# Kernel tuning notes

Hardware: AMD Instinct MI355X
Metric: run time of the kernel (lower is better)

## Reference

```python
import jax, jax.numpy as jnp
import numpy as np

B, S, D, H = 16, 4096, 1024, 1024
VOCAB = 512
EMB_DIM = 3


def setup_inputs() -> dict:
    key = jax.random.key(0)
    ks = jax.random.split(key, 12)
    sd = 1.0 / np.sqrt(D)
    sh = 1.0 / np.sqrt(H)
    return {
        "hs": jax.random.normal(ks[0], (B, S, D), dtype=jnp.float32),
        "ht_k": jax.random.normal(ks[1], (B, D), dtype=jnp.float32),
        "hm_k": jax.random.normal(ks[2], (B, H), dtype=jnp.float32),
        "Ws_w": jax.random.uniform(ks[3], (H, D), jnp.float32, -sd, sd),
        "Ws_b": jax.random.uniform(ks[4], (H,), jnp.float32, -sd, sd),
        "Wt_w": jax.random.uniform(ks[5], (H, D), jnp.float32, -sd, sd),
        "Wt_b": jax.random.uniform(ks[6], (H,), jnp.float32, -sd, sd),
        "Wr_w": jax.random.uniform(ks[7], (H, H), jnp.float32, -sh, sh),
        "Wr_b": jax.random.uniform(ks[8], (H,), jnp.float32, -sh, sh),
        "We_w": jax.random.uniform(ks[9], (H,), jnp.float32, -sh, sh),
        "We_b": jax.random.uniform(ks[10], (1,), jnp.float32, -sh, sh),
        "emb_table": jax.random.normal(ks[11], (VOCAB * VOCAB, EMB_DIM), dtype=jnp.float32),
        "entity_lambda": jnp.array([0.3, 0.5, 0.2], dtype=jnp.float32),
        "hs_i": jax.random.randint(jax.random.fold_in(key, 100), (B, S), 0, VOCAB),
        "ht_k_i": jax.random.randint(jax.random.fold_in(key, 101), (B,), 0, VOCAB),
    }


def reference(hs, ht_k, hm_k, Ws_w, Ws_b, Wt_w, Wt_b, Wr_w, Wr_b, We_w, We_b,
              emb_table, entity_lambda, hs_i, ht_k_i):
    # Projections
    W_hs = jnp.einsum('bsd,hd->bsh', hs, Ws_w) + Ws_b          # [B,S,H]
    W_ht = (ht_k @ Wt_w.T + Wt_b)[:, None, :]                   # [B,1,H]
    W_hm = (hm_k @ Wr_w.T + Wr_b)[:, None, :]                   # [B,1,H]
    # Additive attention score
    W_sum = jnp.tanh(W_hs + W_ht + W_hm) @ We_w + We_b[0]       # [B,S]
    # Relative-position bias: gather then contract with lambda
    rel_pos = hs_i * VOCAB + ht_k_i[:, None]                    # [B,S]
    rel_value = emb_table[rel_pos] @ entity_lambda              # [B,S]
    W_sum = W_sum + rel_value
    # Softmax over sequence, weighted sum of projected source states
    W_softmax = jax.nn.softmax(W_sum, axis=1)                   # [B,S]
    alpha = jnp.einsum('bs,bsh->bh', W_softmax, W_hs)           # [B,H]
    return alpha
```

## Files before the change

### kernel.cpp

```cpp
#include <hip/hip_runtime.h>
#include <hip/hip_bf16.h>
#include <cstdint>
#include <cstddef>

typedef __attribute__((ext_vector_type(4))) float f32x4;
typedef __attribute__((ext_vector_type(8))) short short8;

#define S_LEN 4096
#define D_DIM 1024
#define H_DIM 1024
#define B_SZ  16
#define M_TOT (B_SZ * S_LEN)
#define NT 32

__device__ __forceinline__ unsigned short f2bf(float f) {
  unsigned int u = __float_as_uint(f);
  u += 0x7fffu + ((u >> 16) & 1u);
  return (unsigned short)(u >> 16);
}

__device__ __forceinline__ void gload_lds16(void* lds, const void* g) {
  __builtin_amdgcn_global_load_lds(
      (const __attribute__((address_space(1))) unsigned int*)g,
      (__attribute__((address_space(3))) unsigned int*)lds, 16, 0, 0);
}

__device__ __forceinline__ float tanh_fast(float x) {
  return 1.0f - 2.0f / (1.0f + __expf(2.0f * x));
}

__global__ void cvt_hs_kernel(const float* __restrict__ w,
                              unsigned short* __restrict__ o) {
  size_t i = ((size_t)blockIdx.x * 256 + threadIdx.x) * 8;
  float4 v0 = *(const float4*)(w + i);
  float4 v1 = *(const float4*)(w + i + 4);
  union { unsigned short us[8]; short8 v; } pk;
  pk.us[0] = f2bf(v0.x); pk.us[1] = f2bf(v0.y);
  pk.us[2] = f2bf(v0.z); pk.us[3] = f2bf(v0.w);
  pk.us[4] = f2bf(v1.x); pk.us[5] = f2bf(v1.y);
  pk.us[6] = f2bf(v1.z); pk.us[7] = f2bf(v1.w);
  *(short8*)(o + i) = pk.v;
}

__global__ void cvt_w_kernel(const float* __restrict__ w,
                             unsigned short* __restrict__ o) {
  int i = (blockIdx.x * 256 + threadIdx.x) * 8;
  float4 v0 = *(const float4*)(w + i);
  float4 v1 = *(const float4*)(w + i + 4);
  union { unsigned short us[8]; short8 v; } pk;
  pk.us[0] = f2bf(v0.x); pk.us[1] = f2bf(v0.y);
  pk.us[2] = f2bf(v0.z); pk.us[3] = f2bf(v0.w);
  pk.us[4] = f2bf(v1.x); pk.us[5] = f2bf(v1.y);
  pk.us[6] = f2bf(v1.z); pk.us[7] = f2bf(v1.w);
  *(short8*)(o + i) = pk.v;
}

__global__ void prep_c_kernel(const float* __restrict__ ht,
                              const float* __restrict__ hm,
                              const float* __restrict__ Wt_w,
                              const float* __restrict__ Wt_b,
                              const float* __restrict__ Wr_w,
                              const float* __restrict__ Wr_b,
                              float* __restrict__ cvec) {
  int gw = blockIdx.x * 4 + (threadIdx.x >> 6);
  int lane = threadIdx.x & 63;
  int b = gw >> 10;
  int h = gw & 1023;
  const float* a1 = ht + b * D_DIM;
  const float* w1 = Wt_w + (size_t)h * D_DIM;
  const float* a2 = hm + b * H_DIM;
  const float* w2 = Wr_w + (size_t)h * H_DIM;
  float acc = 0.f;
#pragma unroll
  for (int i = 0; i < 4; ++i) {
    int d = lane * 4 + i * 256;
    float4 x1 = *(const float4*)(a1 + d);
    float4 y1 = *(const float4*)(w1 + d);
    float4 x2 = *(const float4*)(a2 + d);
    float4 y2 = *(const float4*)(w2 + d);
    acc += x1.x * y1.x + x1.y * y1.y + x1.z * y1.z + x1.w * y1.w;
    acc += x2.x * y2.x + x2.y * y2.y + x2.z * y2.z + x2.w * y2.w;
  }
#pragma unroll
  for (int off = 32; off >= 1; off >>= 1) acc += __shfl_xor(acc, off);
  if (lane == 0) cvec[b * H_DIM + h] = acc + Wt_b[h] + Wr_b[h];
}

__device__ __forceinline__ void issue_tile(int kt, int tid,
                                           unsigned short* lA,
                                           unsigned short* lB,
                                           const unsigned short* pA0,
                                           const unsigned short* pA1,
                                           const unsigned short* pB0,
                                           const unsigned short* pB1) {
  int bq = (kt & 3) * 8192;
  size_t ko = (size_t)kt * 32;
  gload_lds16(&lA[bq + tid * 8], pA0 + ko);
  gload_lds16(&lA[bq + 4096 + tid * 8], pA1 + ko);
  gload_lds16(&lB[bq + tid * 8], pB0 + ko);
  gload_lds16(&lB[bq + 4096 + tid * 8], pB1 + ko);
}

__device__ __forceinline__ void compute_tile(const unsigned short* bufA,
                                             const unsigned short* bufB,
                                             const int* aoff, const int* boff,
                                             f32x4 (&acc)[8][4]) {
  short8 bfr[4];
#pragma unroll
  for (int ni = 0; ni < 4; ++ni)
    bfr[ni] = *(const short8*)(bufB + boff[ni]);
  short8 af[4];
#pragma unroll
  for (int mi = 0; mi < 4; ++mi)
    af[mi] = *(const short8*)(bufA + aoff[mi]);
  __builtin_amdgcn_s_setprio(1);
#pragma unroll
  for (int mi = 0; mi < 4; ++mi)
#pragma unroll
    for (int ni = 0; ni < 4; ++ni)
      acc[mi][ni] = __builtin_amdgcn_mfma_f32_16x16x32_bf16(
          af[mi], bfr[ni], acc[mi][ni], 0, 0, 0);
  __builtin_amdgcn_s_setprio(0);
#pragma unroll
  for (int mi = 0; mi < 4; ++mi)
    af[mi] = *(const short8*)(bufA + aoff[4 + mi]);
  __builtin_amdgcn_s_setprio(1);
#pragma unroll
  for (int mi = 0; mi < 4; ++mi)
#pragma unroll
    for (int ni = 0; ni < 4; ++ni)
      acc[4 + mi][ni] = __builtin_amdgcn_mfma_f32_16x16x32_bf16(
          af[mi], bfr[ni], acc[4 + mi][ni], 0, 0, 0);
  __builtin_amdgcn_s_setprio(0);
}

__global__ __launch_bounds__(512, 2) void score_gemm2_kernel(
    const unsigned short* __restrict__ hsb,
    const unsigned short* __restrict__ Wsb,
    const float* __restrict__ cvec,
    const float* __restrict__ We_w,
    float* __restrict__ score_part) {
  extern __shared__ unsigned short dynls[];
  unsigned short* lA = dynls;
  unsigned short* lB = dynls + 4 * 8192;
  __shared__ float scorebuf[4][256];

  const int tid = threadIdx.x;
  const int lane = tid & 63;
  const int wave = tid >> 6;
  const int wm = wave >> 2;
  const int wn = wave & 3;
  const int l15 = lane & 15;
  const int lg = lane >> 4;

  int d = blockIdx.x;
  int tileid = (d & 7) * 128 + (d >> 3);
  const int mtile = tileid >> 2;
  const int nc = tileid & 3;
  const int m0 = mtile * 256;
  const int n0 = nc * 256;
  const int b = m0 >> 12;

  const int r0 = tid >> 2;
  const int r1 = 128 + r0;
  const int sp = tid & 3;
  const int c0 = (sp ^ ((r0 >> 1) & 3)) * 8;
  const int c1 = (sp ^ ((r1 >> 1) & 3)) * 8;
  const unsigned short* pA0 = hsb + (size_t)(m0 + r0) * D_DIM + c0;
  const unsigned short* pA1 = hsb + (size_t)(m0 + r1) * D_DIM + c1;
  const unsigned short* pB0 = Wsb + (size_t)(n0 + r0) * D_DIM + c0;
  const unsigned short* pB1 = Wsb + (size_t)(n0 + r1) * D_DIM + c1;

  int aoff[8], boff[4];
#pragma unroll
  for (int mi = 0; mi < 8; ++mi) {
    int row = wm * 128 + mi * 16 + l15;
    aoff[mi] = row * 32 + (lg ^ ((row >> 1) & 3)) * 8;
  }
#pragma unroll
  for (int ni = 0; ni < 4; ++ni) {
    int row = wn * 64 + ni * 16 + l15;
    boff[ni] = row * 32 + (lg ^ ((row >> 1) & 3)) * 8;
  }

  f32x4 acc[8][4];
#pragma unroll
  for (int i = 0; i < 8; ++i)
#pragma unroll
    for (int j = 0; j < 4; ++j) acc[i][j] = (f32x4){0.f, 0.f, 0.f, 0.f};

  issue_tile(0, tid, lA, lB, pA0, pA1, pB0, pB1);
  issue_tile(1, tid, lA, lB, pA0, pA1, pB0, pB1);
  issue_tile(2, tid, lA, lB, pA0, pA1, pB0, pB1);
  asm volatile("s_waitcnt vmcnt(8)\n\ts_barrier" ::: "memory");

  for (int kt = 0; kt < NT - 3; ++kt) {
    issue_tile(kt + 3, tid, lA, lB, pA0, pA1, pB0, pB1);
    int bq = (kt & 3) * 8192;
    compute_tile(lA + bq, lB + bq, aoff, boff, acc);
    asm volatile("s_waitcnt vmcnt(8)\n\ts_barrier" ::: "memory");
  }
  {
    int bq = ((NT - 3) & 3) * 8192;
    compute_tile(lA + bq, lB + bq, aoff, boff, acc);
    asm volatile("s_waitcnt vmcnt(4)\n\ts_barrier" ::: "memory");
  }
  {
    int bq = ((NT - 2) & 3) * 8192;
    compute_tile(lA + bq, lB + bq, aoff, boff, acc);
    asm volatile("s_waitcnt vmcnt(0)\n\ts_barrier" ::: "memory");
  }
  {
    int bq = ((NT - 1) & 3) * 8192;
    compute_tile(lA + bq, lB + bq, aoff, boff, acc);
  }

  float chv[4], whv[4];
#pragma unroll
  for (int ni = 0; ni < 4; ++ni) {
    int h = n0 + wn * 64 + ni * 16 + l15;
    chv[ni] = cvec[b * H_DIM + h];
    whv[ni] = We_w[h];
  }
#pragma unroll
  for (int mi = 0; mi < 8; ++mi)
#pragma unroll
    for (int r = 0; r < 4; ++r) {
      float s = 0.f;
#pragma unroll
      for (int ni = 0; ni < 4; ++ni)
        s += tanh_fast(acc[mi][ni][r] + chv[ni]) * whv[ni];
      s += __shfl_xor(s, 1);
      s += __shfl_xor(s, 2);
      s += __shfl_xor(s, 4);
      s += __shfl_xor(s, 8);
      if (l15 == 0) scorebuf[wn][wm * 128 + mi * 16 + lg * 4 + r] = s;
    }
  __syncthreads();
  if (tid < 256) {
    float s = scorebuf[0][tid] + scorebuf[1][tid] + scorebuf[2][tid] +
              scorebuf[3][tid];
    score_part[(size_t)nc * M_TOT + m0 + tid] = s;
  }
}

__global__ __launch_bounds__(256) void score_gemm_fp32_kernel(
    const float* __restrict__ hs,
    const unsigned short* __restrict__ Wsb,
    const float* __restrict__ cvec,
    const float* __restrict__ We_w,
    float* __restrict__ score_part) {
  __shared__ __align__(16) unsigned short lA[128 * 64];
  __shared__ __align__(16) unsigned short lB[128 * 64];
  __shared__ float scorebuf[2][128];

  const int tid = threadIdx.x;
  const int lane = tid & 63;
  const int wave = tid >> 6;
  const int wr = wave >> 1;
  const int wc = wave & 1;
  const int mtile = blockIdx.x;
  const int gy = blockIdx.y;
  const int m0 = mtile * 128;
  const int b = mtile >> 5;
  const int l15 = lane & 15;
  const int lg = lane >> 4;

  float rowsum[4][4];
#pragma unroll
  for (int i = 0; i < 4; ++i)
#pragma unroll
    for (int j = 0; j < 4; ++j) rowsum[i][j] = 0.f;

  for (int ncq = gy * 4; ncq < gy * 4 + 4; ++ncq) {
    const int n0 = ncq * 128;
    f32x4 acc[4][4];
#pragma unroll
    for (int i = 0; i < 4; ++i)
#pragma unroll
      for (int j = 0; j < 4; ++j) acc[i][j] = (f32x4){0.f, 0.f, 0.f, 0.f};

    for (int k0 = 0; k0 < D_DIM; k0 += 64) {
#pragma unroll
      for (int r = 0; r < 4; ++r) {
        int s = tid + r * 256;
        int row = s >> 3, sl = s & 7;
        int src = sl ^ (row & 7);
        gload_lds16(&lB[s * 8], Wsb + (size_t)(n0 + row) * D_DIM + k0 + src * 8);
      }
      float4 a0[4], a1[4];
#pragma unroll
      for (int r = 0; r < 4; ++r) {
        int s = tid + r * 256;
        int row = s >> 3, sl = s & 7;
        int src = sl ^ (row & 7);
        const float* ga = hs + (size_t)(m0 + row) * D_DIM + k0 + src * 8;
        a0[r] = *(const float4*)ga;
        a1[r] = *(const float4*)(ga + 4);
      }
#pragma unroll
      for (int r = 0; r < 4; ++r) {
        int s = tid + r * 256;
        union { unsigned short us[8]; short8 v; } pk;
        pk.us[0] = f2bf(a0[r].x); pk.us[1] = f2bf(a0[r].y);
        pk.us[2] = f2bf(a0[r].z); pk.us[3] = f2bf(a0[r].w);
        pk.us[4] = f2bf(a1[r].x); pk.us[5] = f2bf(a1[r].y);
        pk.us[6] = f2bf(a1[r].z); pk.us[7] = f2bf(a1[r].w);
        *(short8*)(&lA[s * 8]) = pk.v;
      }
      __syncthreads();
#pragma unroll
      for (int kf = 0; kf < 2; ++kf) {
        short8 af[4], bfr[4];
        int cgrp = kf * 4 + lg;
#pragma unroll
        for (int mi = 0; mi < 4; ++mi) {
          int row = wr * 64 + mi * 16 + l15;
          af[mi] = *(const short8*)&lA[row * 64 + (cgrp ^ (row & 7)) * 8];
        }
#pragma unroll
        for (int ni = 0; ni < 4; ++ni) {
          int row = wc * 64 + ni * 16 + l15;
          bfr[ni] = *(const short8*)&lB[row * 64 + (cgrp ^ (row & 7)) * 8];
        }
#pragma unroll
        for (int mi = 0; mi < 4; ++mi)
#pragma unroll
          for (int ni = 0; ni < 4; ++ni)
            acc[mi][ni] = __builtin_amdgcn_mfma_f32_16x16x32_bf16(
                af[mi], bfr[ni], acc[mi][ni], 0, 0, 0);
      }
      __syncthreads();
    }
#pragma unroll
    for (int ni = 0; ni < 4; ++ni) {
      int h = n0 + wc * 64 + ni * 16 + l15;
      float ch = cvec[b * H_DIM + h];
      float wh = We_w[h];
#pragma unroll
      for (int mi = 0; mi < 4; ++mi)
#pragma unroll
        for (int r2 = 0; r2 < 4; ++r2)
          rowsum[mi][r2] += tanh_fast(acc[mi][ni][r2] + ch) * wh;
    }
  }
#pragma unroll
  for (int mi = 0; mi < 4; ++mi)
#pragma unroll
    for (int r2 = 0; r2 < 4; ++r2) {
      float v = rowsum[mi][r2];
      v += __shfl_xor(v, 1);
      v += __shfl_xor(v, 2);
      v += __shfl_xor(v, 4);
      v += __shfl_xor(v, 8);
      rowsum[mi][r2] = v;
    }
  if (l15 == 0) {
#pragma unroll
    for (int mi = 0; mi < 4; ++mi)
#pragma unroll
      for (int r2 = 0; r2 < 4; ++r2)
        scorebuf[wc][wr * 64 + mi * 16 + lg * 4 + r2] = rowsum[mi][r2];
  }
  __syncthreads();
  if (tid < 128) {
    score_part[(size_t)gy * M_TOT + m0 + tid] =
        scorebuf[0][tid] + scorebuf[1][tid];
  }
}

__global__ void softmax_kernel(const float* __restrict__ part,
                               const int* __restrict__ hs_i,
                               const int* __restrict__ ht_i,
                               const float* __restrict__ emb,
                               const float* __restrict__ lam,
                               float* __restrict__ wout, int nparts) {
  int b = blockIdx.x;
  int tid = threadIdx.x;
  float lam0 = lam[0], lam1 = lam[1], lam2 = lam[2];
  int tk = ht_i[b];
  float xs[16];
  float mx = -1e30f;
#pragma unroll
  for (int i = 0; i < 16; ++i) {
    int s = tid + i * 256;
    size_t m = (size_t)b * S_LEN + s;
    float x = 0.f;
    for (int g = 0; g < nparts; ++g) x += part[(size_t)g * M_TOT + m];
    int idx = hs_i[m] * 512 + tk;
    const float* e = emb + (size_t)idx * 3;
    x += e[0] * lam0 + e[1] * lam1 + e[2] * lam2;
    xs[i] = x;
    mx = fmaxf(mx, x);
  }
  __shared__ float redm[4];
  __shared__ float reds[4];
#pragma unroll
  for (int off = 32; off >= 1; off >>= 1) mx = fmaxf(mx, __shfl_xor(mx, off));
  if ((tid & 63) == 0) redm[tid >> 6] = mx;
  __syncthreads();
  mx = fmaxf(fmaxf(redm[0], redm[1]), fmaxf(redm[2], redm[3]));
  float sum = 0.f;
#pragma unroll
  for (int i = 0; i < 16; ++i) {
    xs[i] = __expf(xs[i] - mx);
    sum += xs[i];
  }
#pragma unroll
  for (int off = 32; off >= 1; off >>= 1) sum += __shfl_xor(sum, off);
  if ((tid & 63) == 0) reds[tid >> 6] = sum;
  __syncthreads();
  sum = reds[0] + reds[1] + reds[2] + reds[3];
  float inv = 1.0f / sum;
#pragma unroll
  for (int i = 0; i < 16; ++i)
    wout[(size_t)b * S_LEN + tid + i * 256] = xs[i] * inv;
}

__global__ void wsum_bf16_kernel(const unsigned short* __restrict__ hsb,
                                 const float* __restrict__ w,
                                 float* __restrict__ u) {
  int bx = blockIdx.x;
  int b = bx >> 5;
  int sc = bx & 31;
  int tid = threadIdx.x;
  int dcol = tid * 4;
  int s0 = sc * 128;
  const unsigned short* base = hsb + ((size_t)b * S_LEN + s0) * D_DIM + dcol;
  const float* wrow = w + (size_t)b * S_LEN + s0;
  float4 acc = {0.f, 0.f, 0.f, 0.f};
#pragma unroll 4
  for (int i = 0; i < 128; ++i) {
    float ww = wrow[i];
    ushort2 v01 = *(const ushort2*)(base + (size_t)i * D_DIM);
    ushort2 v23 = *(const ushort2*)(base + (size_t)i * D_DIM + 2);
    acc.x += ww * __uint_as_float((unsigned int)v01.x << 16);
    acc.y += ww * __uint_as_float((unsigned int)v01.y << 16);
    acc.z += ww * __uint_as_float((unsigned int)v23.x << 16);
    acc.w += ww * __uint_as_float((unsigned int)v23.y << 16);
  }
  atomicAdd(&u[b * D_DIM + dcol + 0], acc.x);
  atomicAdd(&u[b * D_DIM + dcol + 1], acc.y);
  atomicAdd(&u[b * D_DIM + dcol + 2], acc.z);
  atomicAdd(&u[b * D_DIM + dcol + 3], acc.w);
}

__global__ void wsum_kernel(const float* __restrict__ hs,
                            const float* __restrict__ w,
                            float* __restrict__ u) {
  int bx = blockIdx.x;
  int b = bx >> 5;
  int sc = bx & 31;
  int tid = threadIdx.x;
  int dcol = tid * 4;
  int s0 = sc * 128;
  const float* base = hs + ((size_t)b * S_LEN + s0) * D_DIM + dcol;
  const float* wrow = w + (size_t)b * S_LEN + s0;
  float4 acc = {0.f, 0.f, 0.f, 0.f};
#pragma unroll 4
  for (int i = 0; i < 128; ++i) {
    float ww = wrow[i];
    float4 v = *(const float4*)(base + (size_t)i * D_DIM);
    acc.x += ww * v.x;
    acc.y += ww * v.y;
    acc.z += ww * v.z;
    acc.w += ww * v.w;
  }
  atomicAdd(&u[b * D_DIM + dcol + 0], acc.x);
  atomicAdd(&u[b * D_DIM + dcol + 1], acc.y);
  atomicAdd(&u[b * D_DIM + dcol + 2], acc.z);
  atomicAdd(&u[b * D_DIM + dcol + 3], acc.w);
}

__global__ void alpha_kernel(const float* __restrict__ u,
                             const float* __restrict__ Ws_w,
                             const float* __restrict__ Ws_b,
                             float* __restrict__ out) {
  int gw = blockIdx.x * 4 + (threadIdx.x >> 6);
  int lane = threadIdx.x & 63;
  int b = gw >> 10;
  int h = gw & 1023;
  const float* ur = u + b * D_DIM;
  const float* wrow = Ws_w + (size_t)h * D_DIM;
  float acc = 0.f;
#pragma unroll
  for (int i = 0; i < 4; ++i) {
    int dcol = lane * 4 + i * 256;
    float4 x = *(const float4*)(ur + dcol);
    float4 y = *(const float4*)(wrow + dcol);
    acc += x.x * y.x + x.y * y.y + x.z * y.z + x.w * y.w;
  }
#pragma unroll
  for (int off = 32; off >= 1; off >>= 1) acc += __shfl_xor(acc, off);
  if (lane == 0) out[b * H_DIM + h] = acc + Ws_b[h];
}

extern "C" void kernel_launch(void* const* d_in, const int* in_sizes, int n_in,
                              void* d_out, int out_size, void* d_ws,
                              size_t ws_size, hipStream_t stream) {
  const float* hs = (const float*)d_in[0];
  const float* ht_k = (const float*)d_in[1];
  const float* hm_k = (const float*)d_in[2];
  const float* Ws_w = (const float*)d_in[3];
  const float* Ws_b = (const float*)d_in[4];
  const float* Wt_w = (const float*)d_in[5];
  const float* Wt_b = (const float*)d_in[6];
  const float* Wr_w = (const float*)d_in[7];
  const float* Wr_b = (const float*)d_in[8];
  const float* We_w = (const float*)d_in[9];
  const float* emb = (const float*)d_in[11];
  const float* lam = (const float*)d_in[12];
  const int* hs_i = (const int*)d_in[13];
  const int* ht_i = (const int*)d_in[14];
  float* out = (float*)d_out;

  const size_t HSB = (size_t)M_TOT * D_DIM * 2;
  const size_t FAST_NEEDED = HSB + 2097152 + 1048576 + 262144 + 65536 + 65536;

  char* ws = (char*)d_ws;
  if (ws_size >= FAST_NEEDED) {
    unsigned short* hsb = (unsigned short*)ws;
    unsigned short* Wsb = (unsigned short*)(ws + HSB);
    float* part = (float*)(ws + HSB + 2097152);
    float* wgt = (float*)(ws + HSB + 2097152 + 1048576);
    float* u = (float*)(ws + HSB + 2097152 + 1048576 + 262144);
    float* cvec = (float*)(ws + HSB + 2097152 + 1048576 + 262144 + 65536);

    hipFuncSetAttribute((const void*)score_gemm2_kernel,
                        hipFuncAttributeMaxDynamicSharedMemorySize, 131072);

    cvt_hs_kernel<<<32768, 256, 0, stream>>>(hs, hsb);
    cvt_w_kernel<<<512, 256, 0, stream>>>(Ws_w, Wsb);
    prep_c_kernel<<<4096, 256, 0, stream>>>(ht_k, hm_k, Wt_w, Wt_b, Wr_w,
                                            Wr_b, cvec);
    score_gemm2_kernel<<<1024, 512, 131072, stream>>>(hsb, Wsb, cvec, We_w,
                                                      part);
    softmax_kernel<<<16, 256, 0, stream>>>(part, hs_i, ht_i, emb, lam, wgt, 4);
    hipMemsetAsync(u, 0, B_SZ * D_DIM * sizeof(float), stream);
    wsum_bf16_kernel<<<512, 256, 0, stream>>>(hsb, wgt, u);
    alpha_kernel<<<4096, 256, 0, stream>>>(u, Ws_w, Ws_b, out);
    return;
  }

  unsigned short* Wsb = (unsigned short*)(ws);
  float* cvec = (float*)(ws + 2097152);
  float* part = (float*)(ws + 2097152 + 65536);
  float* wgt = (float*)(ws + 2097152 + 65536 + 524288);
  float* u = (float*)(ws + 2097152 + 65536 + 524288 + 262144);

  cvt_w_kernel<<<512, 256, 0, stream>>>(Ws_w, Wsb);
  prep_c_kernel<<<4096, 256, 0, stream>>>(ht_k, hm_k, Wt_w, Wt_b, Wr_w, Wr_b,
                                          cvec);
  dim3 g2(512, 2);
  score_gemm_fp32_kernel<<<g2, 256, 0, stream>>>(hs, Wsb, cvec, We_w, part);
  softmax_kernel<<<16, 256, 0, stream>>>(part, hs_i, ht_i, emb, lam, wgt, 2);
  hipMemsetAsync(u, 0, B_SZ * D_DIM * sizeof(float), stream);
  wsum_kernel<<<512, 256, 0, stream>>>(hs, wgt, u);
  alpha_kernel<<<4096, 256, 0, stream>>>(u, Ws_w, Ws_b, out);
}
```

Before: 303.2 us.

## Double-buffer LDS fragment reads in registers to overlap with MFMA

Restructures the score GEMM main loop so the LDS fragments for the next k-tile are read into a second register set while MFMAs run on the current set. The loop is unrolled by two, and global-to-LDS prefetch issue and waitcnt/barrier placement are reshuffled so each stage waits on only one outstanding tile. Per-fragment offset arrays are replaced with a base offset plus constant strides. This aims to hide LDS read latency behind matrix math, at the cost of roughly doubling fragment register usage, which risks spills or lower occupancy under the 512x2 launch bound.

```diff
diff --git a/kernel.cpp b/kernel.cpp
--- a/kernel.cpp
+++ b/kernel.cpp
@@ -28,6 +28,9 @@
 __device__ __forceinline__ float tanh_fast(float x) {
   return 1.0f - 2.0f / (1.0f + __expf(2.0f * x));
 }
+
+#define WAITV(N) asm volatile("s_waitcnt vmcnt(" #N ")" ::: "memory")
+#define BAR() __builtin_amdgcn_s_barrier()
 
 __global__ void cvt_hs_kernel(const float* __restrict__ w,
                               unsigned short* __restrict__ o) {
@@ -93,44 +96,36 @@
                                            const unsigned short* pA1,
                                            const unsigned short* pB0,
                                            const unsigned short* pB1) {
-  int bq = (kt & 3) * 8192;
-  size_t ko = (size_t)kt * 32;
+  const int bq = (kt & 3) * 8192;
+  const int ko = kt * 32;
   gload_lds16(&lA[bq + tid * 8], pA0 + ko);
   gload_lds16(&lA[bq + 4096 + tid * 8], pA1 + ko);
   gload_lds16(&lB[bq + tid * 8], pB0 + ko);
   gload_lds16(&lB[bq + 4096 + tid * 8], pB1 + ko);
 }
 
-__device__ __forceinline__ void compute_tile(const unsigned short* bufA,
-                                             const unsigned short* bufB,
-                                             const int* aoff, const int* boff,
-                                             f32x4 (&acc)[8][4]) {
-  short8 bfr[4];
+__device__ __forceinline__ void read_frags(const unsigned short* bufA,
+                                           const unsigned short* bufB,
+                                           int aoff0, int boff0,
+                                           short8 (&fa)[8], short8 (&fb)[4]) {
 #pragma unroll
   for (int ni = 0; ni < 4; ++ni)
-    bfr[ni] = *(const short8*)(bufB + boff[ni]);
-  short8 af[4];
-#pragma unroll
-  for (int mi = 0; mi < 4; ++mi)
-    af[mi] = *(const short8*)(bufA + aoff[mi]);
+    fb[ni] = *(const short8*)(bufB + boff0 + ni * 512);
+#pragma unroll
+  for (int mi = 0; mi < 8; ++mi)
+    fa[mi] = *(const short8*)(bufA + aoff0 + mi * 512);
+}
+
+__device__ __forceinline__ void mfma32(const short8 (&fa)[8],
+                                       const short8 (&fb)[4],
+                                       f32x4 (&acc)[8][4]) {
   __builtin_amdgcn_s_setprio(1);
 #pragma unroll
-  for (int mi = 0; mi < 4; ++mi)
+  for (int mi = 0; mi < 8; ++mi)
 #pragma unroll
     for (int ni = 0; ni < 4; ++ni)
       acc[mi][ni] = __builtin_amdgcn_mfma_f32_16x16x32_bf16(
-          af[mi], bfr[ni], acc[mi][ni], 0, 0, 0);
-  __builtin_amdgcn_s_setprio(0);
-#pragma unroll
-  for (int mi = 0; mi < 4; ++mi)
-    af[mi] = *(const short8*)(bufA + aoff[4 + mi]);
-  __builtin_amdgcn_s_setprio(1);
-#pragma unroll
-  for (int mi = 0; mi < 4; ++mi)
-#pragma unroll
-    for (int ni = 0; ni < 4; ++ni)
-      acc[4 + mi][ni] = __builtin_amdgcn_mfma_f32_16x16x32_bf16(
-          af[mi], bfr[ni], acc[4 + mi][ni], 0, 0, 0);
+          fa[mi], fb[ni], acc[mi][ni], 0, 0, 0);
   __builtin_amdgcn_s_setprio(0);
 }
 
@@ -142,7 +137,7 @@
     float* __restrict__ score_part) {
   extern __shared__ unsigned short dynls[];
   unsigned short* lA = dynls;
-  unsigned short* lB = dynls + 4 * 8192;
+  unsigned short* lB = dynls + 32768;
   __shared__ float scorebuf[4][256];
 
   const int tid = threadIdx.x;
@@ -171,49 +166,65 @@
   const unsigned short* pB0 = Wsb + (size_t)(n0 + r0) * D_DIM + c0;
   const unsigned short* pB1 = Wsb + (size_t)(n0 + r1) * D_DIM + c1;
 
-  int aoff[8], boff[4];
-#pragma unroll
-  for (int mi = 0; mi < 8; ++mi) {
-    int row = wm * 128 + mi * 16 + l15;
-    aoff[mi] = row * 32 + (lg ^ ((row >> 1) & 3)) * 8;
-  }
-#pragma unroll
-  for (int ni = 0; ni < 4; ++ni) {
-    int row = wn * 64 + ni * 16 + l15;
-    boff[ni] = row * 32 + (lg ^ ((row >> 1) & 3)) * 8;
-  }
+  const int arow0 = wm * 128 + l15;
+  const int aoff0 = arow0 * 32 + (lg ^ ((arow0 >> 1) & 3)) * 8;
+  const int brow0 = wn * 64 + l15;
+  const int boff0 = brow0 * 32 + (lg ^ ((brow0 >> 1) & 3)) * 8;
 
   f32x4 acc[8][4];
 #pragma unroll
   for (int i = 0; i < 8; ++i)
 #pragma unroll
     for (int j = 0; j < 4; ++j) acc[i][j] = (f32x4){0.f, 0.f, 0.f, 0.f};
+
+  short8 fa0[8], fb0[4], fa1[8], fb1[4];
 
   issue_tile(0, tid, lA, lB, pA0, pA1, pB0, pB1);
   issue_tile(1, tid, lA, lB, pA0, pA1, pB0, pB1);
   issue_tile(2, tid, lA, lB, pA0, pA1, pB0, pB1);
-  asm volatile("s_waitcnt vmcnt(8)\n\ts_barrier" ::: "memory");
-
-  for (int kt = 0; kt < NT - 3; ++kt) {
+  WAITV(4);
+  BAR();
+  read_frags(lA, lB, aoff0, boff0, fa0, fb0);
+
+  for (int kt = 0; kt < NT - 4; kt += 2) {
     issue_tile(kt + 3, tid, lA, lB, pA0, pA1, pB0, pB1);
-    int bq = (kt & 3) * 8192;
-    compute_tile(lA + bq, lB + bq, aoff, boff, acc);
-    asm volatile("s_waitcnt vmcnt(8)\n\ts_barrier" ::: "memory");
-  }
+    {
+      int bq = ((kt + 1) & 3) * 8192;
+      read_frags(lA + bq, lB + bq, aoff0, boff0, fa1, fb1);
+    }
+    mfma32(fa0, fb0, acc);
+    WAITV(4);
+    BAR();
+    issue_tile(kt + 4, tid, lA, lB, pA0, pA1, pB0, pB1);
+    {
+      int bq = ((kt + 2) & 3) * 8192;
+      read_frags(lA + bq, lB + bq, aoff0, boff0, fa0, fb0);
+    }
+    mfma32(fa1, fb1, acc);
+    WAITV(4);
+    BAR();
+  }
+  issue_tile(NT - 1, tid, lA, lB, pA0, pA1, pB0, pB1);
   {
     int bq = ((NT - 3) & 3) * 8192;
-    compute_tile(lA + bq, lB + bq, aoff, boff, acc);
-    asm volatile("s_waitcnt vmcnt(4)\n\ts_barrier" ::: "memory");
-  }
+    read_frags(lA + bq, lB + bq, aoff0, boff0, fa1, fb1);
+  }
+  mfma32(fa0, fb0, acc);
+  WAITV(4);
+  BAR();
   {
     int bq = ((NT - 2) & 3) * 8192;
-    compute_tile(lA + bq, lB + bq, aoff, boff, acc);
-    asm volatile("s_waitcnt vmcnt(0)\n\ts_barrier" ::: "memory");
-  }
+    read_frags(lA + bq, lB + bq, aoff0, boff0, fa0, fb0);
+  }
+  mfma32(fa1, fb1, acc);
+  WAITV(0);
+  BAR();
   {
     int bq = ((NT - 1) & 3) * 8192;
-    compute_tile(lA + bq, lB + bq, aoff, boff, acc);
-  }
+    read_frags(lA + bq, lB + bq, aoff0, boff0, fa1, fb1);
+  }
+  mfma32(fa0, fb0, acc);
+  mfma32(fa1, fb1, acc);
 
   float chv[4], whv[4];
 #pragma unroll
```

Result: no change. 299.3 us (-1.3%).

## Replace 256x256 four-stage score GEMM with 128x128 double-buffered tiles

Applied to the files above, without the earlier changes.

Replaces the 256x256-tile, 512-thread score GEMM, which used a 4-deep global-to-LDS pipeline and 128KB of dynamic shared memory, with a 128x128-tile, 256-thread kernel. The new kernel uses static double-buffered LDS and a simple issue-next/compute/wait loop. The smaller tile allows more blocks per CU and drops the dynamic-shared-memory attribute setup. In exchange it halves per-block operand reuse, which doubles global/L2 traffic for the bf16 GEMM. The score partials grow from 4 to 8 N-chunks, so the workspace and the softmax reduction count are enlarged to match.

```diff
diff --git a/kernel.cpp b/kernel.cpp
--- a/kernel.cpp
+++ b/kernel.cpp
@@ -11,7 +11,6 @@
 #define H_DIM 1024
 #define B_SZ  16
 #define M_TOT (B_SZ * S_LEN)
-#define NT 32
 
 __device__ __forceinline__ unsigned short f2bf(float f) {
   unsigned int u = __float_as_uint(f);
@@ -28,6 +27,9 @@
 __device__ __forceinline__ float tanh_fast(float x) {
   return 1.0f - 2.0f / (1.0f + __expf(2.0f * x));
 }
+
+#define BAR() __builtin_amdgcn_s_barrier()
+#define WAITV0() asm volatile("s_waitcnt vmcnt(0)" ::: "memory")
 
 __global__ void cvt_hs_kernel(const float* __restrict__ w,
                               unsigned short* __restrict__ o) {
@@ -86,144 +88,101 @@
   if (lane == 0) cvec[b * H_DIM + h] = acc + Wt_b[h] + Wr_b[h];
 }
 
-__device__ __forceinline__ void issue_tile(int kt, int tid,
-                                           unsigned short* lA,
-                                           unsigned short* lB,
-                                           const unsigned short* pA0,
-                                           const unsigned short* pA1,
-                                           const unsigned short* pB0,
-                                           const unsigned short* pB1) {
-  int bq = (kt & 3) * 8192;
-  size_t ko = (size_t)kt * 32;
-  gload_lds16(&lA[bq + tid * 8], pA0 + ko);
-  gload_lds16(&lA[bq + 4096 + tid * 8], pA1 + ko);
-  gload_lds16(&lB[bq + tid * 8], pB0 + ko);
-  gload_lds16(&lB[bq + 4096 + tid * 8], pB1 + ko);
-}
-
-__device__ __forceinline__ void compute_tile(const unsigned short* bufA,
-                                             const unsigned short* bufB,
-                                             const int* aoff, const int* boff,
-                                             f32x4 (&acc)[8][4]) {
-  short8 bfr[4];
-#pragma unroll
-  for (int ni = 0; ni < 4; ++ni)
-    bfr[ni] = *(const short8*)(bufB + boff[ni]);
-  short8 af[4];
-#pragma unroll
-  for (int mi = 0; mi < 4; ++mi)
-    af[mi] = *(const short8*)(bufA + aoff[mi]);
-  __builtin_amdgcn_s_setprio(1);
-#pragma unroll
-  for (int mi = 0; mi < 4; ++mi)
-#pragma unroll
-    for (int ni = 0; ni < 4; ++ni)
-      acc[mi][ni] = __builtin_amdgcn_mfma_f32_16x16x32_bf16(
-          af[mi], bfr[ni], acc[mi][ni], 0, 0, 0);
-  __builtin_amdgcn_s_setprio(0);
-#pragma unroll
-  for (int mi = 0; mi < 4; ++mi)
-    af[mi] = *(const short8*)(bufA + aoff[4 + mi]);
-  __builtin_amdgcn_s_setprio(1);
-#pragma unroll
-  for (int mi = 0; mi < 4; ++mi)
-#pragma unroll
-    for (int ni = 0; ni < 4; ++ni)
-      acc[4 + mi][ni] = __builtin_amdgcn_mfma_f32_16x16x32_bf16(
-          af[mi], bfr[ni], acc[4 + mi][ni], 0, 0, 0);
-  __builtin_amdgcn_s_setprio(0);
-}
-
-__global__ __launch_bounds__(512, 2) void score_gemm2_kernel(
+__global__ __launch_bounds__(256, 4) void score_gemm4_kernel(
     const unsigned short* __restrict__ hsb,
     const unsigned short* __restrict__ Wsb,
     const float* __restrict__ cvec,
     const float* __restrict__ We_w,
     float* __restrict__ score_part) {
-  extern __shared__ unsigned short dynls[];
-  unsigned short* lA = dynls;
-  unsigned short* lB = dynls + 4 * 8192;
-  __shared__ float scorebuf[4][256];
+  __shared__ __align__(16) unsigned short lA[2][4096];
+  __shared__ __align__(16) unsigned short lB[2][4096];
+  __shared__ float scorebuf[2][128];
 
   const int tid = threadIdx.x;
   const int lane = tid & 63;
   const int wave = tid >> 6;
-  const int wm = wave >> 2;
-  const int wn = wave & 3;
+  const int wr = wave >> 1;
+  const int wc = wave & 1;
   const int l15 = lane & 15;
   const int lg = lane >> 4;
 
   int d = blockIdx.x;
-  int tileid = (d & 7) * 128 + (d >> 3);
-  const int mtile = tileid >> 2;
-  const int nc = tileid & 3;
-  const int m0 = mtile * 256;
-  const int n0 = nc * 256;
+  int tileid = (d & 7) * 512 + (d >> 3);
+  const int mtile = tileid >> 3;
+  const int nc = tileid & 7;
+  const int m0 = mtile * 128;
+  const int n0 = nc * 128;
   const int b = m0 >> 12;
 
   const int r0 = tid >> 2;
-  const int r1 = 128 + r0;
-  const int sp = tid & 3;
-  const int c0 = (sp ^ ((r0 >> 1) & 3)) * 8;
-  const int c1 = (sp ^ ((r1 >> 1) & 3)) * 8;
+  const int r1 = 64 + r0;
+  const int sl = tid & 3;
+  const int c0 = ((sl ^ ((r0 >> 1) & 3)) << 3);
+  const int c1 = ((sl ^ ((r1 >> 1) & 3)) << 3);
   const unsigned short* pA0 = hsb + (size_t)(m0 + r0) * D_DIM + c0;
   const unsigned short* pA1 = hsb + (size_t)(m0 + r1) * D_DIM + c1;
   const unsigned short* pB0 = Wsb + (size_t)(n0 + r0) * D_DIM + c0;
   const unsigned short* pB1 = Wsb + (size_t)(n0 + r1) * D_DIM + c1;
-
-  int aoff[8], boff[4];
-#pragma unroll
-  for (int mi = 0; mi < 8; ++mi) {
-    int row = wm * 128 + mi * 16 + l15;
-    aoff[mi] = row * 32 + (lg ^ ((row >> 1) & 3)) * 8;
-  }
+  const int dst0 = tid * 8;
+  const int dst1 = 2048 + tid * 8;
+
+  const int arow = wr * 64 + l15;
+  const int aoff = arow * 32 + ((lg ^ ((arow >> 1) & 3)) << 3);
+  const int brow = wc * 64 + l15;
+  const int boff = brow * 32 + ((lg ^ ((brow >> 1) & 3)) << 3);
+
+  f32x4 acc[4][4];
+#pragma unroll
+  for (int i = 0; i < 4; ++i)
+#pragma unroll
+    for (int j = 0; j < 4; ++j) acc[i][j] = (f32x4){0.f, 0.f, 0.f, 0.f};
+
+#define ISSUE4(SB, KO)                          \
+  do {                                          \
+    gload_lds16(&lA[SB][dst0], pA0 + (KO));     \
+    gload_lds16(&lA[SB][dst1], pA1 + (KO));     \
+    gload_lds16(&lB[SB][dst0], pB0 + (KO));     \
+    gload_lds16(&lB[SB][dst1], pB1 + (KO));     \
+  } while (0)
+
+  ISSUE4(0, 0);
+  WAITV0();
+  BAR();
+
+#pragma unroll 2
+  for (int s = 0; s < 32; ++s) {
+    if (s < 31) ISSUE4((s + 1) & 1, (s + 1) * 32);
+    const unsigned short* bA = lA[s & 1];
+    const unsigned short* bB = lB[s & 1];
+    short8 fa[4], fb[4];
+#pragma unroll
+    for (int ni = 0; ni < 4; ++ni)
+      fb[ni] = *(const short8*)(bB + boff + ni * 512);
+#pragma unroll
+    for (int mi = 0; mi < 4; ++mi)
+      fa[mi] = *(const short8*)(bA + aoff + mi * 512);
+    __builtin_amdgcn_s_setprio(1);
+#pragma unroll
+    for (int mi = 0; mi < 4; ++mi)
+#pragma unroll
+      for (int ni = 0; ni < 4; ++ni)
+        acc[mi][ni] = __builtin_amdgcn_mfma_f32_16x16x32_bf16(
+            fa[mi], fb[ni], acc[mi][ni], 0, 0, 0);
+    __builtin_amdgcn_s_setprio(0);
+    WAITV0();
+    BAR();
+  }
+#undef ISSUE4
+
+  float chv[4], whv[4];
 #pragma unroll
   for (int ni = 0; ni < 4; ++ni) {
-    int row = wn * 64 + ni * 16 + l15;
-    boff[ni] = row * 32 + (lg ^ ((row >> 1) & 3)) * 8;
-  }
-
-  f32x4 acc[8][4];
-#pragma unroll
-  for (int i = 0; i < 8; ++i)
-#pragma unroll
-    for (int j = 0; j < 4; ++j) acc[i][j] = (f32x4){0.f, 0.f, 0.f, 0.f};
-
-  issue_tile(0, tid, lA, lB, pA0, pA1, pB0, pB1);
-  issue_tile(1, tid, lA, lB, pA0, pA1, pB0, pB1);
-  issue_tile(2, tid, lA, lB, pA0, pA1, pB0, pB1);
-  asm volatile("s_waitcnt vmcnt(8)\n\ts_barrier" ::: "memory");
-
-  for (int kt = 0; kt < NT - 3; ++kt) {
-    issue_tile(kt + 3, tid, lA, lB, pA0, pA1, pB0, pB1);
-    int bq = (kt & 3) * 8192;
-    compute_tile(lA + bq, lB + bq, aoff, boff, acc);
-    asm volatile("s_waitcnt vmcnt(8)\n\ts_barrier" ::: "memory");
-  }
-  {
-    int bq = ((NT - 3) & 3) * 8192;
-    compute_tile(lA + bq, lB + bq, aoff, boff, acc);
-    asm volatile("s_waitcnt vmcnt(4)\n\ts_barrier" ::: "memory");
-  }
-  {
-    int bq = ((NT - 2) & 3) * 8192;
-    compute_tile(lA + bq, lB + bq, aoff, boff, acc);
-    asm volatile("s_waitcnt vmcnt(0)\n\ts_barrier" ::: "memory");
-  }
-  {
-    int bq = ((NT - 1) & 3) * 8192;
-    compute_tile(lA + bq, lB + bq, aoff, boff, acc);
-  }
-
-  float chv[4], whv[4];
-#pragma unroll
-  for (int ni = 0; ni < 4; ++ni) {
-    int h = n0 + wn * 64 + ni * 16 + l15;
+    int h = n0 + wc * 64 + ni * 16 + l15;
     chv[ni] = cvec[b * H_DIM + h];
     whv[ni] = We_w[h];
   }
 #pragma unroll
-  for (int mi = 0; mi < 8; ++mi)
+  for (int mi = 0; mi < 4; ++mi)
 #pragma unroll
     for (int r = 0; r < 4; ++r) {
       float s = 0.f;
@@ -234,13 +193,12 @@
       s += __shfl_xor(s, 2);
       s += __shfl_xor(s, 4);
       s += __shfl_xor(s, 8);
-      if (l15 == 0) scorebuf[wn][wm * 128 + mi * 16 + lg * 4 + r] = s;
+      if (l15 == 0) scorebuf[wc][wr * 64 + mi * 16 + lg * 4 + r] = s;
     }
   __syncthreads();
-  if (tid < 256) {
-    float s = scorebuf[0][tid] + scorebuf[1][tid] + scorebuf[2][tid] +
-              scorebuf[3][tid];
-    score_part[(size_t)nc * M_TOT + m0 + tid] = s;
+  if (tid < 128) {
+    score_part[(size_t)nc * M_TOT + m0 + tid] =
+        scorebuf[0][tid] + scorebuf[1][tid];
   }
 }
 
@@ -284,16 +242,16 @@
 #pragma unroll
       for (int r = 0; r < 4; ++r) {
         int s = tid + r * 256;
-        int row = s >> 3, sl = s & 7;
-        int src = sl ^ (row & 7);
+        int row = s >> 3, slx = s & 7;
+        int src = slx ^ (row & 7);
         gload_lds16(&lB[s * 8], Wsb + (size_t)(n0 + row) * D_DIM + k0 + src * 8);
       }
       float4 a0[4], a1[4];
 #pragma unroll
       for (int r = 0; r < 4; ++r) {
         int s = tid + r * 256;
-        int row = s >> 3, sl = s & 7;
-        int src = sl ^ (row & 7);
+        int row = s >> 3, slx = s & 7;
+        int src = slx ^ (row & 7);
         const float* ga = hs + (size_t)(m0 + row) * D_DIM + k0 + src * 8;
         a0[r] = *(const float4*)ga;
         a1[r] = *(const float4*)(ga + 4);
@@ -515,27 +473,24 @@
   float* out = (float*)d_out;
 
   const size_t HSB = (size_t)M_TOT * D_DIM * 2;
-  const size_t FAST_NEEDED = HSB + 2097152 + 1048576 + 262144 + 65536 + 65536;
+  const size_t FAST_NEEDED =
+      HSB + 2097152 + 2097152 + 262144 + 65536 + 65536;
 
   char* ws = (char*)d_ws;
   if (ws_size >= FAST_NEEDED) {
     unsigned short* hsb = (unsigned short*)ws;
     unsigned short* Wsb = (unsigned short*)(ws + HSB);
     float* part = (float*)(ws + HSB + 2097152);
-    float* wgt = (float*)(ws + HSB + 2097152 + 1048576);
-    float* u = (float*)(ws + HSB + 2097152 + 1048576 + 262144);
-    float* cvec = (float*)(ws + HSB + 2097152 + 1048576 + 262144 + 65536);
-
-    hipFuncSetAttribute((const void*)score_gemm2_kernel,
-                        hipFuncAttributeMaxDynamicSharedMemorySize, 131072);
+    float* wgt = (float*)(ws + HSB + 2097152 + 2097152);
+    float* u = (float*)(ws + HSB + 2097152 + 2097152 + 262144);
+    float* cvec = (float*)(ws + HSB + 2097152 + 2097152 + 262144 + 65536);
 
     cvt_hs_kernel<<<32768, 256, 0, stream>>>(hs, hsb);
     cvt_w_kernel<<<512, 256, 0, stream>>>(Ws_w, Wsb);
     prep_c_kernel<<<4096, 256, 0, stream>>>(ht_k, hm_k, Wt_w, Wt_b, Wr_w,
                                             Wr_b, cvec);
-    score_gemm2_kernel<<<1024, 512, 131072, stream>>>(hsb, Wsb, cvec, We_w,
-                                                      part);
-    softmax_kernel<<<16, 256, 0, stream>>>(part, hs_i, ht_i, emb, lam, wgt, 4);
+    score_gemm4_kernel<<<4096, 256, 0, stream>>>(hsb, Wsb, cvec, We_w, part);
+    softmax_kernel<<<16, 256, 0, stream>>>(part, hs_i, ht_i, emb, lam, wgt, 8);
     hipMemsetAsync(u, 0, B_SZ * D_DIM * sizeof(float), stream);
     wsum_bf16_kernel<<<512, 256, 0, stream>>>(hsb, wgt, u);
     alpha_kernel<<<4096, 256, 0, stream>>>(u, Ws_w, Ws_b, out);
```

Result: slower. 334.5 us (+10.3%).
